# Performance work log

Hardware: AMD Instinct MI355X
Metric: run time of the kernel (lower is better)

## Reference

```python
import jax, jax.numpy as jnp
import numpy as np

ALPHA = 0.2       # LeakyReLU negative slope
NEG_INF = -9e15   # matches torch's -9000000000000000.0 masking constant


def setup_inputs() -> dict:
    key = jax.random.key(0)
    k1, k2, k3, k4 = jax.random.split(key, 4)
    N, Cin, T, V = 16, 64, 512, 64   # in_channels == out_channels == V == C (forced by module math)
    x = jax.random.normal(k1, (N, Cin, T, V), dtype=jnp.float32)
    # K=3 adjacency partitions with 0/1 entries; forward sums over dim 0 and masks where sum > 0
    A = jax.random.randint(k2, (3, V, V), 0, 2).astype(jnp.float32)
    # learned params (xavier-ish scale)
    W = jax.random.normal(k3, (V, V), dtype=jnp.float32) * 0.15
    a = jax.random.normal(k4, (2 * Cin, 1), dtype=jnp.float32) * 0.15
    return {"x": x, "A": A, "W": W, "a": a}


def reference(x, A, W, a):
    # x: [N, C, T, V_in]; W contracts the vertex dim (last axis), as in torch.matmul(x, W)
    x = jnp.einsum('nctv,vu->nctu', x, W)
    N, C, T, V = x.shape
    xf = x.transpose(0, 2, 3, 1).reshape(N * T, V, C)   # [B, V, C], B = N*T
    Asum = jnp.sum(A, axis=0)                           # [V, V]
    # e[b,i,j] = leakyrelu(cat(x_i, x_j) @ a) = leakyrelu(x_i@a1 + x_j@a2)
    a1, a2 = a[:C, 0], a[C:, 0]                         # [C], [C]
    f = xf @ a1                                         # [B, V]
    g = xf @ a2                                         # [B, V]
    e = jax.nn.leaky_relu(f[:, :, None] + g[:, None, :], ALPHA)  # [B, V, V]
    att = jnp.where(Asum[None, :, :] > 0, e, NEG_INF)
    att = jax.nn.softmax(att, axis=2)
    # dropout is identity in eval mode
    out = jnp.einsum('bij,bjc->bic', att, xf)           # [B, V, C]
    return out.reshape(N, T, V, C).transpose(0, 3, 1, 2)  # [N, C, T, V]
```

## Files before the change

kernel.cpp:

```cpp
#include <hip/hip_runtime.h>
#include <hip/hip_bf16.h>


using bf16x8 = __attribute__((ext_vector_type(8))) short;
using f32x4  = __attribute__((ext_vector_type(4))) float;

constexpr float ALPHA = 0.2f;

__device__ __forceinline__ unsigned short f2bf(float f) {
    union { __hip_bfloat16 h; unsigned short s; } u;
    u.h = __float2bfloat16(f);
    return u.s;
}

__global__ void mask_kernel(const float* __restrict__ A,
                            unsigned long long* __restrict__ mask) {
    const int i = threadIdx.x;
    unsigned long long m = 0;
    for (int j = 0; j < 64; ++j) {
        float s = A[i*64 + j] + A[4096 + i*64 + j] + A[8192 + i*64 + j];
        if (s > 0.f) m |= (1ull << j);
    }
    mask[i] = m;
}

__global__ __launch_bounds__(256, 6) void gat_kernel(
    const float* __restrict__ x,
    const float* __restrict__ a,
    const unsigned long long* __restrict__ maskbits,
    const float* __restrict__ W,
    float* __restrict__ out)
{
    __shared__ unsigned short XbYb[64 * 72];
    __shared__ unsigned short WtPb[64 * 72];
    __shared__ float al[128];
    __shared__ float fpart[4][64];
    __shared__ float gpart[4][64];
    __shared__ unsigned long long ml[64];

    const int tid  = threadIdx.x;
    const int b    = blockIdx.x;
    const int n    = b >> 9, t = b & 511;
    const int w    = tid >> 6, lane = tid & 63;
    const int fr   = lane & 15;
    const int hi   = lane >> 4;
    const int fk   = hi * 8;

    {
        const int c = tid >> 2, q = tid & 3;
        const float* xp = x + (size_t)n * 2097152 + (size_t)c * 32768 + (size_t)t * 64 + q * 16;
        float4 v0 = ((const float4*)xp)[0];
        float4 v1 = ((const float4*)xp)[1];
        float4 v2 = ((const float4*)xp)[2];
        float4 v3 = ((const float4*)xp)[3];
        union { bf16x8 v; unsigned short s[8]; } u0, u1;
        u0.s[0]=f2bf(v0.x); u0.s[1]=f2bf(v0.y); u0.s[2]=f2bf(v0.z); u0.s[3]=f2bf(v0.w);
        u0.s[4]=f2bf(v1.x); u0.s[5]=f2bf(v1.y); u0.s[6]=f2bf(v1.z); u0.s[7]=f2bf(v1.w);
        u1.s[0]=f2bf(v2.x); u1.s[1]=f2bf(v2.y); u1.s[2]=f2bf(v2.z); u1.s[3]=f2bf(v2.w);
        u1.s[4]=f2bf(v3.x); u1.s[5]=f2bf(v3.y); u1.s[6]=f2bf(v3.z); u1.s[7]=f2bf(v3.w);
        *(bf16x8*)&XbYb[c * 72 + q * 16]     = u0.v;
        *(bf16x8*)&XbYb[c * 72 + q * 16 + 8] = u1.v;
    }
    {
        const int u = tid >> 2;
        #pragma unroll
        for (int rep = 0; rep < 4; ++rep) {
            const int c4 = (tid & 3) + 4 * rep;
            float4 wv = *(const float4*)&W[u * 64 + c4 * 4];
            WtPb[(c4 * 4 + 0) * 72 + u] = f2bf(wv.x);
            WtPb[(c4 * 4 + 1) * 72 + u] = f2bf(wv.y);
            WtPb[(c4 * 4 + 2) * 72 + u] = f2bf(wv.z);
            WtPb[(c4 * 4 + 3) * 72 + u] = f2bf(wv.w);
        }
    }
    if (tid < 128) al[tid] = a[tid];
    if (tid >= 192) ml[tid - 192] = maskbits[tid - 192];
    __syncthreads();

    {
        f32x4 acc[4] = {{0,0,0,0},{0,0,0,0},{0,0,0,0},{0,0,0,0}};
        #pragma unroll
        for (int kc = 0; kc < 2; ++kc) {
            bf16x8 af = *(const bf16x8*)&XbYb[(16 * w + fr) * 72 + 32 * kc + fk];
            #pragma unroll
            for (int cb = 0; cb < 4; ++cb) {
                bf16x8 bfr = *(const bf16x8*)&WtPb[(16 * cb + fr) * 72 + 32 * kc + fk];
                acc[cb] = __builtin_amdgcn_mfma_f32_16x16x32_bf16(af, bfr, acc[cb], 0, 0, 0);
            }
        }
        float a1r[4], a2r[4];
        #pragma unroll
        for (int r = 0; r < 4; ++r) {
            a1r[r] = al[16 * w + 4 * hi + r];
            a2r[r] = al[64 + 16 * w + 4 * hi + r];
        }
        #pragma unroll
        for (int cb = 0; cb < 4; ++cb) {
            #pragma unroll
            for (int r = 0; r < 4; ++r)
                XbYb[(16 * w + 4 * hi + r) * 72 + 16 * cb + fr] = f2bf(acc[cb][r]);
            float F = acc[cb][0]*a1r[0] + acc[cb][1]*a1r[1] + acc[cb][2]*a1r[2] + acc[cb][3]*a1r[3];
            float G = acc[cb][0]*a2r[0] + acc[cb][1]*a2r[1] + acc[cb][2]*a2r[2] + acc[cb][3]*a2r[3];
            F += __shfl_xor(F, 16, 64); F += __shfl_xor(F, 32, 64);
            G += __shfl_xor(G, 16, 64); G += __shfl_xor(G, 32, 64);
            if (lane < 16) {
                fpart[w][16 * cb + lane] = F;
                gpart[w][16 * cb + lane] = G;
            }
        }
    }
    __syncthreads();

    {
        const float gj = (gpart[0][lane] + gpart[1][lane]) + (gpart[2][lane] + gpart[3][lane]);
        #pragma unroll 4
        for (int k = 0; k < 16; ++k) {
            const int i = 4 * k + w;
            const unsigned long long mi = ml[i];
            const float fi = (fpart[0][i] + fpart[1][i]) + (fpart[2][i] + fpart[3][i]);
            const float s0 = fi + gj;
            const float e  = fmaxf(s0, ALPHA * s0);
            float p;
            if (mi == 0ull) p = 1.0f;
            else            p = ((mi >> lane) & 1ull) ? __expf(e) : 0.0f;
            WtPb[i * 72 + lane] = f2bf(p);
        }
    }
    __syncthreads();

    {
        f32x4 acc2[4] = {{0,0,0,0},{0,0,0,0},{0,0,0,0},{0,0,0,0}};
        f32x4 accS[4] = {{0,0,0,0},{0,0,0,0},{0,0,0,0},{0,0,0,0}};
        union { bf16x8 v; unsigned short s[8]; } ones;
        #pragma unroll
        for (int j = 0; j < 8; ++j) ones.s[j] = 0x3f80;
        #pragma unroll
        for (int kc = 0; kc < 2; ++kc) {
            bf16x8 af = *(const bf16x8*)&XbYb[(16 * w + fr) * 72 + 32 * kc + fk];
            #pragma unroll
            for (int cb = 0; cb < 4; ++cb) {
                bf16x8 bfr = *(const bf16x8*)&WtPb[(16 * cb + fr) * 72 + 32 * kc + fk];
                acc2[cb] = __builtin_amdgcn_mfma_f32_16x16x32_bf16(af, bfr, acc2[cb], 0, 0, 0);
                accS[cb] = __builtin_amdgcn_mfma_f32_16x16x32_bf16(ones.v, bfr, accS[cb], 0, 0, 0);
            }
        }
        float* op = out + (size_t)n * 2097152 + (size_t)t * 64;
        #pragma unroll
        for (int cb = 0; cb < 4; ++cb) {
            const float rs  = __builtin_amdgcn_rcpf(accS[cb][0]);
            const int   col = 16 * cb + fr;
            #pragma unroll
            for (int r = 0; r < 4; ++r) {
                const int row = 16 * w + 4 * hi + r;
                op[(size_t)row * 32768 + col] = acc2[cb][r] * rs;
            }
        }
    }
}

extern "C" void kernel_launch(void* const* d_in, const int* in_sizes, int n_in,
                              void* d_out, int out_size, void* d_ws, size_t ws_size,
                              hipStream_t stream) {
    const float* x = (const float*)d_in[0];
    const float* A = (const float*)d_in[1];
    const float* W = (const float*)d_in[2];
    const float* a = (const float*)d_in[3];
    float* out = (float*)d_out;
    unsigned long long* mask = (unsigned long long*)d_ws;

    mask_kernel<<<1, 64, 0, stream>>>(A, mask);
    gat_kernel<<<16 * 512, 256, 0, stream>>>(x, a, mask, W, out);
}
```

Measured before the change: 54.56 us.

## Precompute bf16 transposed W once, load MFMA operands directly into registers

```diff
diff --git a/kernel.cpp b/kernel.cpp
--- a/kernel.cpp
+++ b/kernel.cpp
@@ -4,8 +4,10 @@
 
 using bf16x8 = __attribute__((ext_vector_type(8))) short;
 using f32x4  = __attribute__((ext_vector_type(4))) float;
+typedef unsigned long long ull;
 
 constexpr float ALPHA = 0.2f;
+constexpr float LOG2E = 1.4426950408889634f;
 
 __device__ __forceinline__ unsigned short f2bf(float f) {
     union { __hip_bfloat16 h; unsigned short s; } u;
@@ -13,100 +15,88 @@
     return u.s;
 }
 
-__global__ void mask_kernel(const float* __restrict__ A,
-                            unsigned long long* __restrict__ mask) {
-    const int i = threadIdx.x;
-    unsigned long long m = 0;
-    for (int j = 0; j < 64; ++j) {
-        float s = A[i*64 + j] + A[4096 + i*64 + j] + A[8192 + i*64 + j];
-        if (s > 0.f) m |= (1ull << j);
+__global__ void prep_kernel(const float* __restrict__ A,
+                            const float* __restrict__ W,
+                            unsigned short* __restrict__ Wt,
+                            ull* __restrict__ mask) {
+    const int tid = threadIdx.x;
+    const int v = tid & 63, q = tid >> 6;
+    #pragma unroll 4
+    for (int m = 0; m < 16; ++m) {
+        const int u = 16 * q + m;
+        Wt[v * 64 + u] = f2bf(W[u * 64 + v]);
     }
-    mask[i] = m;
+    if (tid < 64) {
+        ull m = 0;
+        for (int j = 0; j < 64; ++j) {
+            float s = A[tid * 64 + j] + A[4096 + tid * 64 + j] + A[8192 + tid * 64 + j];
+            if (s > 0.f) m |= (1ull << j);
+        }
+        mask[tid] = m;
+    }
 }
 
-__global__ __launch_bounds__(256, 6) void gat_kernel(
+__global__ __launch_bounds__(256, 4) void gat_kernel(
     const float* __restrict__ x,
     const float* __restrict__ a,
-    const unsigned long long* __restrict__ maskbits,
-    const float* __restrict__ W,
+    const unsigned short* __restrict__ Wt,
+    const ull* __restrict__ maskbits,
     float* __restrict__ out)
 {
-    __shared__ unsigned short XbYb[64 * 72];
-    __shared__ unsigned short WtPb[64 * 72];
-    __shared__ float al[128];
+    __shared__ unsigned short Yl[64 * 72];
+    __shared__ unsigned short Pl[64 * 72];
     __shared__ float fpart[4][64];
     __shared__ float gpart[4][64];
-    __shared__ unsigned long long ml[64];
+    __shared__ ull ml[64];
 
-    const int tid  = threadIdx.x;
-    const int b    = blockIdx.x;
-    const int n    = b >> 9, t = b & 511;
-    const int w    = tid >> 6, lane = tid & 63;
-    const int fr   = lane & 15;
-    const int hi   = lane >> 4;
-    const int fk   = hi * 8;
+    const int tid = threadIdx.x;
+    const int b = blockIdx.x;
+    const int n = b >> 9, t = b & 511;
+    const int w = tid >> 6, lane = tid & 63;
+    const int fr = lane & 15, hi = lane >> 4;
 
-    {
-        const int c = tid >> 2, q = tid & 3;
-        const float* xp = x + (size_t)n * 2097152 + (size_t)c * 32768 + (size_t)t * 64 + q * 16;
-        float4 v0 = ((const float4*)xp)[0];
-        float4 v1 = ((const float4*)xp)[1];
-        float4 v2 = ((const float4*)xp)[2];
-        float4 v3 = ((const float4*)xp)[3];
-        union { bf16x8 v; unsigned short s[8]; } u0, u1;
-        u0.s[0]=f2bf(v0.x); u0.s[1]=f2bf(v0.y); u0.s[2]=f2bf(v0.z); u0.s[3]=f2bf(v0.w);
-        u0.s[4]=f2bf(v1.x); u0.s[5]=f2bf(v1.y); u0.s[6]=f2bf(v1.z); u0.s[7]=f2bf(v1.w);
-        u1.s[0]=f2bf(v2.x); u1.s[1]=f2bf(v2.y); u1.s[2]=f2bf(v2.z); u1.s[3]=f2bf(v2.w);
-        u1.s[4]=f2bf(v3.x); u1.s[5]=f2bf(v3.y); u1.s[6]=f2bf(v3.z); u1.s[7]=f2bf(v3.w);
-        *(bf16x8*)&XbYb[c * 72 + q * 16]     = u0.v;
-        *(bf16x8*)&XbYb[c * 72 + q * 16 + 8] = u1.v;
+    if (tid < 64) ml[tid] = maskbits[tid];
+
+    const float* xr = x + (size_t)n * 2097152 + (size_t)(16 * w + fr) * 32768
+                        + (size_t)t * 64;
+    bf16x8 af[2];
+    #pragma unroll
+    for (int kc = 0; kc < 2; ++kc) {
+        float4 l0 = *(const float4*)(xr + 32 * kc + 8 * hi);
+        float4 l1 = *(const float4*)(xr + 32 * kc + 8 * hi + 4);
+        union { bf16x8 v; unsigned short s[8]; } u;
+        u.s[0] = f2bf(l0.x); u.s[1] = f2bf(l0.y); u.s[2] = f2bf(l0.z); u.s[3] = f2bf(l0.w);
+        u.s[4] = f2bf(l1.x); u.s[5] = f2bf(l1.y); u.s[6] = f2bf(l1.z); u.s[7] = f2bf(l1.w);
+        af[kc] = u.v;
     }
-    {
-        const int u = tid >> 2;
+    bf16x8 bw[4][2];
+    #pragma unroll
+    for (int cb = 0; cb < 4; ++cb)
         #pragma unroll
-        for (int rep = 0; rep < 4; ++rep) {
-            const int c4 = (tid & 3) + 4 * rep;
-            float4 wv = *(const float4*)&W[u * 64 + c4 * 4];
-            WtPb[(c4 * 4 + 0) * 72 + u] = f2bf(wv.x);
-            WtPb[(c4 * 4 + 1) * 72 + u] = f2bf(wv.y);
-            WtPb[(c4 * 4 + 2) * 72 + u] = f2bf(wv.z);
-            WtPb[(c4 * 4 + 3) * 72 + u] = f2bf(wv.w);
-        }
-    }
-    if (tid < 128) al[tid] = a[tid];
-    if (tid >= 192) ml[tid - 192] = maskbits[tid - 192];
-    __syncthreads();
+        for (int kc = 0; kc < 2; ++kc)
+            bw[cb][kc] = *(const bf16x8*)&Wt[(16 * cb + fr) * 64 + 32 * kc + 8 * hi];
 
-    {
-        f32x4 acc[4] = {{0,0,0,0},{0,0,0,0},{0,0,0,0},{0,0,0,0}};
+    f32x4 acc[4] = {{0,0,0,0},{0,0,0,0},{0,0,0,0},{0,0,0,0}};
+    #pragma unroll
+    for (int kc = 0; kc < 2; ++kc)
         #pragma unroll
-        for (int kc = 0; kc < 2; ++kc) {
-            bf16x8 af = *(const bf16x8*)&XbYb[(16 * w + fr) * 72 + 32 * kc + fk];
-            #pragma unroll
-            for (int cb = 0; cb < 4; ++cb) {
-                bf16x8 bfr = *(const bf16x8*)&WtPb[(16 * cb + fr) * 72 + 32 * kc + fk];
-                acc[cb] = __builtin_amdgcn_mfma_f32_16x16x32_bf16(af, bfr, acc[cb], 0, 0, 0);
-            }
-        }
-        float a1r[4], a2r[4];
+        for (int cb = 0; cb < 4; ++cb)
+            acc[cb] = __builtin_amdgcn_mfma_f32_16x16x32_bf16(af[kc], bw[cb][kc], acc[cb], 0, 0, 0);
+
+    const float4 a1v = *(const float4*)&a[16 * w + 4 * hi];
+    const float4 a2v = *(const float4*)&a[64 + 16 * w + 4 * hi];
+    #pragma unroll
+    for (int cb = 0; cb < 4; ++cb) {
         #pragma unroll
-        for (int r = 0; r < 4; ++r) {
-            a1r[r] = al[16 * w + 4 * hi + r];
-            a2r[r] = al[64 + 16 * w + 4 * hi + r];
-        }
-        #pragma unroll
-        for (int cb = 0; cb < 4; ++cb) {
-            #pragma unroll
-            for (int r = 0; r < 4; ++r)
-                XbYb[(16 * w + 4 * hi + r) * 72 + 16 * cb + fr] = f2bf(acc[cb][r]);
-            float F = acc[cb][0]*a1r[0] + acc[cb][1]*a1r[1] + acc[cb][2]*a1r[2] + acc[cb][3]*a1r[3];
-            float G = acc[cb][0]*a2r[0] + acc[cb][1]*a2r[1] + acc[cb][2]*a2r[2] + acc[cb][3]*a2r[3];
-            F += __shfl_xor(F, 16, 64); F += __shfl_xor(F, 32, 64);
-            G += __shfl_xor(G, 16, 64); G += __shfl_xor(G, 32, 64);
-            if (lane < 16) {
-                fpart[w][16 * cb + lane] = F;
-                gpart[w][16 * cb + lane] = G;
-            }
+        for (int r = 0; r < 4; ++r)
+            Yl[(16 * w + 4 * hi + r) * 72 + 16 * cb + fr] = f2bf(acc[cb][r]);
+        float F = acc[cb][0]*a1v.x + acc[cb][1]*a1v.y + acc[cb][2]*a1v.z + acc[cb][3]*a1v.w;
+        float G = acc[cb][0]*a2v.x + acc[cb][1]*a2v.y + acc[cb][2]*a2v.z + acc[cb][3]*a2v.w;
+        F += __shfl_xor(F, 16, 64); F += __shfl_xor(F, 32, 64);
+        G += __shfl_xor(G, 16, 64); G += __shfl_xor(G, 32, 64);
+        if (lane < 16) {
+            fpart[w][16 * cb + lane] = F * LOG2E;
+            gpart[w][16 * cb + lane] = G * LOG2E;
         }
     }
     __syncthreads();
@@ -115,47 +105,43 @@
         const float gj = (gpart[0][lane] + gpart[1][lane]) + (gpart[2][lane] + gpart[3][lane]);
         #pragma unroll 4
         for (int k = 0; k < 16; ++k) {
-            const int i = 4 * k + w;
-            const unsigned long long mi = ml[i];
+            const int i = 16 * w + k;
+            const ull mi = ml[i];
             const float fi = (fpart[0][i] + fpart[1][i]) + (fpart[2][i] + fpart[3][i]);
             const float s0 = fi + gj;
-            const float e  = fmaxf(s0, ALPHA * s0);
-            float p;
-            if (mi == 0ull) p = 1.0f;
-            else            p = ((mi >> lane) & 1ull) ? __expf(e) : 0.0f;
-            WtPb[i * 72 + lane] = f2bf(p);
+            const float e = fmaxf(s0, ALPHA * s0);
+            const float p = (mi == 0ull) ? 1.0f
+                          : (((mi >> lane) & 1ull) ? exp2f(e) : 0.0f);
+            Pl[i * 72 + lane] = f2bf(p);
         }
     }
-    __syncthreads();
+    asm volatile("s_waitcnt lgkmcnt(0)" ::: "memory");
 
-    {
-        f32x4 acc2[4] = {{0,0,0,0},{0,0,0,0},{0,0,0,0},{0,0,0,0}};
-        f32x4 accS[4] = {{0,0,0,0},{0,0,0,0},{0,0,0,0},{0,0,0,0}};
-        union { bf16x8 v; unsigned short s[8]; } ones;
+    bf16x8 pb0 = *(const bf16x8*)&Pl[(16 * w + fr) * 72 + 8 * hi];
+    bf16x8 pb1 = *(const bf16x8*)&Pl[(16 * w + fr) * 72 + 32 + 8 * hi];
+    union { bf16x8 v; unsigned short s[8]; } ones;
+    #pragma unroll
+    for (int j = 0; j < 8; ++j) ones.s[j] = 0x3f80;
+    f32x4 accS = {0, 0, 0, 0};
+    accS = __builtin_amdgcn_mfma_f32_16x16x32_bf16(ones.v, pb0, accS, 0, 0, 0);
+    accS = __builtin_amdgcn_mfma_f32_16x16x32_bf16(ones.v, pb1, accS, 0, 0, 0);
+
+    f32x4 acc2[4] = {{0,0,0,0},{0,0,0,0},{0,0,0,0},{0,0,0,0}};
+    #pragma unroll
+    for (int rb = 0; rb < 4; ++rb) {
+        bf16x8 y0 = *(const bf16x8*)&Yl[(16 * rb + fr) * 72 + 8 * hi];
+        bf16x8 y1 = *(const bf16x8*)&Yl[(16 * rb + fr) * 72 + 32 + 8 * hi];
+        acc2[rb] = __builtin_amdgcn_mfma_f32_16x16x32_bf16(y0, pb0, acc2[rb], 0, 0, 0);
+        acc2[rb] = __builtin_amdgcn_mfma_f32_16x16x32_bf16(y1, pb1, acc2[rb], 0, 0, 0);
+    }
+    const float rs = __builtin_amdgcn_rcpf(accS[0]);
+    float* op = out + (size_t)n * 2097152 + (size_t)t * 64 + 16 * w + fr;
+    #pragma unroll
+    for (int rb = 0; rb < 4; ++rb)
         #pragma unroll
-        for (int j = 0; j < 8; ++j) ones.s[j] = 0x3f80;
-        #pragma unroll
-        for (int kc = 0; kc < 2; ++kc) {
-            bf16x8 af = *(const bf16x8*)&XbYb[(16 * w + fr) * 72 + 32 * kc + fk];
-            #pragma unroll
-            for (int cb = 0; cb < 4; ++cb) {
-                bf16x8 bfr = *(const bf16x8*)&WtPb[(16 * cb + fr) * 72 + 32 * kc + fk];
-                acc2[cb] = __builtin_amdgcn_mfma_f32_16x16x32_bf16(af, bfr, acc2[cb], 0, 0, 0);
-                accS[cb] = __builtin_amdgcn_mfma_f32_16x16x32_bf16(ones.v, bfr, accS[cb], 0, 0, 0);
-            }
-        }
-        float* op = out + (size_t)n * 2097152 + (size_t)t * 64;
-        #pragma unroll
-        for (int cb = 0; cb < 4; ++cb) {
-            const float rs  = __builtin_amdgcn_rcpf(accS[cb][0]);
-            const int   col = 16 * cb + fr;
-            #pragma unroll
-            for (int r = 0; r < 4; ++r) {
-                const int row = 16 * w + 4 * hi + r;
-                op[(size_t)row * 32768 + col] = acc2[cb][r] * rs;
-            }
-        }
-    }
+        for (int r = 0; r < 4; ++r)
+            __builtin_nontemporal_store(acc2[rb][r] * rs,
+                op + (size_t)(16 * rb + 4 * hi + r) * 32768);
 }
 
 extern "C" void kernel_launch(void* const* d_in, const int* in_sizes, int n_in,
@@ -166,8 +152,9 @@
     const float* W = (const float*)d_in[2];
     const float* a = (const float*)d_in[3];
     float* out = (float*)d_out;
-    unsigned long long* mask = (unsigned long long*)d_ws;
+    unsigned short* Wt = (unsigned short*)d_ws;
+    ull* mask = (ull*)((char*)d_ws + 8192);
 
-    mask_kernel<<<1, 64, 0, stream>>>(A, mask);
-    gat_kernel<<<16 * 512, 256, 0, stream>>>(x, a, mask, W, out);
+    prep_kernel<<<1, 256, 0, stream>>>(A, W, Wt, mask);
+    gat_kernel<<<16 * 512, 256, 0, stream>>>(x, a, Wt, mask, out);
 }
```

Result: slower. 68.23 us (+25.0%).
